# Optimization experiments

Measured on AMD Instinct MI355X. Metric: run time of the kernel, lower is better.

Reference implementation:

```python
import jax, jax.numpy as jnp
import numpy as np

WH, WW = 7, 7
SH, SW = 3, 3
NUM_HEADS = 8


def _rel_pos_index(wh, ww):
    coords = np.stack(np.meshgrid(np.arange(wh), np.arange(ww), indexing='ij')).reshape(2, -1)
    rel = (coords[:, :, None] - coords[:, None, :]).transpose(1, 2, 0)  # [N,N,2]
    rel[..., 0] += wh - 1
    rel[..., 1] += ww - 1
    rel[..., 0] *= 2 * ww - 1
    return rel.sum(-1)  # [N,N] int


def _attn_mask(Hp, Wp, wh, ww, sh, sw):
    img = np.zeros((Hp, Wp), dtype=np.float32)
    cnt = 0
    for hs in (slice(0, -wh), slice(-wh, -sh), slice(-sh, None)):
        for ws in (slice(0, -ww), slice(-ww, -sw), slice(-sw, None)):
            img[hs, ws] = cnt
            cnt += 1
    win = img.reshape(Hp // wh, wh, Wp // ww, ww).transpose(0, 2, 1, 3).reshape(-1, wh * ww)  # [nW,N]
    diff = win[:, None, :] - win[:, :, None]  # [nW,N,N]
    return np.where(diff != 0, -100.0, 0.0).astype(np.float32)


def _layernorm(x, g, b, eps=1e-5):
    mu = jnp.mean(x, -1, keepdims=True)
    var = jnp.mean(jnp.square(x - mu), -1, keepdims=True)
    return (x - mu) * jax.lax.rsqrt(var + eps) * g + b


def setup_inputs() -> dict:
    key = jax.random.key(0)
    ks = jax.random.split(key, 12)
    B, H, W, C = 32, 56, 56, 256
    hid = 4 * C
    s = lambda k, *shape: jax.random.normal(k, shape, jnp.float32) * 0.02
    return {
        'x': jax.random.normal(ks[0], (B, H * W, C), jnp.float32),
        'g1': jnp.ones((C,), jnp.float32), 'b1': jnp.zeros((C,), jnp.float32),
        'qkv_w': s(ks[1], 3 * C, C), 'qkv_b': jnp.zeros((3 * C,), jnp.float32),
        'bias_table': s(ks[2], (2 * WH - 1) * (2 * WW - 1), NUM_HEADS),
        'proj_w': s(ks[3], C, C), 'proj_b': jnp.zeros((C,), jnp.float32),
        'g2': jnp.ones((C,), jnp.float32), 'b2': jnp.zeros((C,), jnp.float32),
        'w1': s(ks[4], hid, C), 'bm1': jnp.zeros((hid,), jnp.float32),
        'w2': s(ks[5], C, hid), 'bm2': jnp.zeros((C,), jnp.float32),
        'H': H, 'W': W,
    }


def reference(x, g1, b1, qkv_w, qkv_b, bias_table, proj_w, proj_b, g2, b2, w1, bm1, w2, bm2, H, W):
    B, L, C = x.shape
    wh, ww = WH, WW
    nH = NUM_HEADS
    hd = C // nH
    scale = hd ** -0.5
    N = wh * ww

    shortcut = x
    h = _layernorm(x, g1, b1).reshape(B, H, W, C)
    pad_b = (wh - H % wh) % wh
    pad_r = (ww - W % ww) % ww
    if pad_b or pad_r:
        h = jnp.pad(h, ((0, 0), (0, pad_b), (0, pad_r), (0, 0)))
    Hp, Wp = h.shape[1], h.shape[2]

    h = jnp.roll(h, (-SH, -SW), axis=(1, 2))
    # window partition -> [B*nW, N, C]
    nWh, nWw = Hp // wh, Wp // ww
    xw = h.reshape(B, nWh, wh, nWw, ww, C).transpose(0, 1, 3, 2, 4, 5).reshape(-1, N, C)

    qkv = jnp.einsum('bnc,oc->bno', xw, qkv_w) + qkv_b  # [B*nW, N, 3C]
    qkv = qkv.reshape(-1, N, 3, nH, hd).transpose(2, 0, 3, 1, 4)
    q, k, v = qkv[0] * scale, qkv[1], qkv[2]  # [B*nW, nH, N, hd]
    attn = jnp.einsum('whnd,whmd->whnm', q, k)  # [B*nW, nH, N, N]

    rpi = jnp.asarray(_rel_pos_index(wh, ww))
    bias = bias_table[rpi.reshape(-1)].reshape(N, N, nH).transpose(2, 0, 1)  # [nH,N,N]
    attn = attn + bias[None]

    mask = jnp.asarray(_attn_mask(Hp, Wp, wh, ww, SH, SW))  # [nW,N,N]
    nW = mask.shape[0]
    attn = attn.reshape(B, nW, nH, N, N) + mask[None, :, None]
    attn = jax.nn.softmax(attn.reshape(-1, nH, N, N), axis=-1)

    out = jnp.einsum('whnm,whmd->whnd', attn, v).transpose(0, 2, 1, 3).reshape(-1, N, C)
    out = jnp.einsum('bnc,oc->bno', out, proj_w) + proj_b

    # window reverse
    out = out.reshape(B, nWh, nWw, wh, ww, C).transpose(0, 1, 3, 2, 4, 5).reshape(B, Hp, Wp, C)
    out = jnp.roll(out, (SH, SW), axis=(1, 2))
    if pad_b or pad_r:
        out = out[:, :H, :W, :]
    out = out.reshape(B, H * W, C)

    x = shortcut + out
    m = _layernorm(x, g2, b2)
    m = jax.nn.gelu(jnp.einsum('blc,oc->blo', m, w1) + bm1, approximate=False)
    m = jnp.einsum('blh,oh->blo', m, w2) + bm2
    return x + m
```

## Files before the change

kernel.cpp:

```cpp
#include <hip/hip_runtime.h>
#include <hip/hip_bf16.h>

#define DEVI __device__ __forceinline__
#define AS1 __attribute__((address_space(1)))
#define AS3 __attribute__((address_space(3)))

typedef short bf16x8 __attribute__((ext_vector_type(8)));
typedef float f32x4  __attribute__((ext_vector_type(4)));
typedef unsigned short u16x4 __attribute__((ext_vector_type(4)));

constexpr int MROWS = 100352;

DEVI int win_row_to_token(int r) {
  int b   = r / 3136;
  int rem = r - b * 3136;
  int wi  = rem / 49;
  int t   = rem - wi * 49;
  int nwh = wi >> 3, nww = wi & 7;
  int th = t / 7, tw = t - th * 7;
  int h = nwh * 7 + th + 3; if (h >= 56) h -= 56;
  int w = nww * 7 + tw + 3; if (w >= 56) w -= 56;
  return b * 3136 + h * 56 + w;
}

DEVI unsigned short f2bf(float f) {
  __hip_bfloat16 h = __float2bfloat16(f);
  return __builtin_bit_cast(unsigned short, h);
}

DEVI float gelu_t(float v) {
  float u2 = v * (1.5957691216f + 0.1426930877f * v * v);
  float e  = __expf(u2);
  return v * e / (e + 1.0f);
}

__global__ void pack_kernel(const float* __restrict__ W, __hip_bfloat16* __restrict__ Wp,
                            int N, int K) {
  long t = (long)blockIdx.x * 256 + threadIdx.x;
  long total = (long)N * K / 8;
  if (t >= total) return;
  int l  = (int)(t & 63);
  long f = t >> 6;
  int ni = (int)(f & 3);
  int kk = (int)((f >> 2) & 7);
  long r = f >> 5;
  int KB = K / 256;
  int kb = (int)(r % KB);
  int nb = (int)(r / KB);
  int row  = nb * 64 + (l & 15) + ni * 16;
  int col0 = kb * 256 + kk * 32 + (l >> 4) * 8;
  const float* src = W + (size_t)row * K + col0;
  u16x4 lo, hi;
  #pragma unroll
  for (int e = 0; e < 4; ++e) { lo[e] = f2bf(src[e]); hi[e] = f2bf(src[4 + e]); }
  *(u16x4*)(Wp + t * 8)     = lo;
  *(u16x4*)(Wp + t * 8 + 4) = hi;
}

__global__ __launch_bounds__(256) void ln_kernel(
    const float* __restrict__ xin, const float* __restrict__ g,
    const float* __restrict__ b, __hip_bfloat16* __restrict__ outb)
{
  int r = blockIdx.x * 4 + (threadIdx.x >> 6);
  int l = threadIdx.x & 63;
  int tok = win_row_to_token(r);
  float4 xv = *(const float4*)&xin[(size_t)tok * 256 + l * 4];
  float s = xv.x + xv.y + xv.z + xv.w;
  float q = xv.x * xv.x + xv.y * xv.y + xv.z * xv.z + xv.w * xv.w;
  #pragma unroll
  for (int off = 32; off; off >>= 1) { s += __shfl_xor(s, off); q += __shfl_xor(q, off); }
  float mu = s * (1.0f / 256.0f);
  float var = q * (1.0f / 256.0f) - mu * mu;
  float rs = rsqrtf(var + 1e-5f);
  float4 gv = *(const float4*)&g[l * 4];
  float4 bv = *(const float4*)&b[l * 4];
  ushort4 st;
  st.x = f2bf((xv.x - mu) * rs * gv.x + bv.x);
  st.y = f2bf((xv.y - mu) * rs * gv.y + bv.y);
  st.z = f2bf((xv.z - mu) * rs * gv.z + bv.z);
  st.w = f2bf((xv.w - mu) * rs * gv.w + bv.w);
  *(ushort4*)&outb[(size_t)r * 256 + l * 4] = st;
}

__global__ __launch_bounds__(256, 3) void gemm_qkv(
    const __hip_bfloat16* __restrict__ A,
    const __hip_bfloat16* __restrict__ Wp,
    const float* __restrict__ bias,
    __hip_bfloat16* __restrict__ outb)
{
  constexpr int CB = 3;
  __shared__ __align__(16) __hip_bfloat16 Al[64 * 256];

  const int tid = threadIdx.x;
  const int w = tid >> 6, l = tid & 63;
  const int g = l >> 4, lm = l & 15;

  const int nwg = gridDim.x;
  int bswz = (blockIdx.x & 7) * (nwg >> 3) + (blockIdx.x >> 3);
  const int mt = bswz / CB;
  const int cb = bswz - mt * CB;

  const char* At = (const char*)A + (size_t)mt * 64 * 512;
  char* AlB = (char*)Al;
  const int r0  = tid >> 5;
  const int usw = ((tid & 31) ^ r0) << 4;
  const int lmx = lm & 7;
  const int arow = lm * 512;

  const __hip_bfloat16* WpB = Wp + (size_t)(cb * 4 + w) * 16384;
  const int colb = cb * 256 + w * 64 + g * 4;

  f32x4 acc[4][4];
  {
    f32x4 bias_v[4];
    #pragma unroll
    for (int ni = 0; ni < 4; ++ni) bias_v[ni] = *(const f32x4*)&bias[colb + ni * 16];
    #pragma unroll
    for (int mi = 0; mi < 4; ++mi)
      #pragma unroll
      for (int ni = 0; ni < 4; ++ni) acc[mi][ni] = bias_v[ni];
  }

  #pragma unroll
  for (int j = 0; j < 8; ++j)
    __builtin_amdgcn_global_load_lds(
        (const AS1 void*)(At + (long)(j * 8 + r0) * 512 + usw),
        (AS3 void*)(AlB + j * 4096 + w * 1024), 16, 0, 0);
  asm volatile("s_waitcnt vmcnt(0)" ::: "memory");
  __syncthreads();

  #pragma unroll
  for (int kk = 0; kk < 8; ++kk) {
    bf16x8 bf[4], af[4];
    #pragma unroll
    for (int ni = 0; ni < 4; ++ni)
      bf[ni] = *(const bf16x8*)(WpB + ((kk * 4 + ni) * 64 + l) * 8);
    #pragma unroll
    for (int mi = 0; mi < 4; ++mi)
      af[mi] = *(const bf16x8*)(AlB + arow + mi * 8192 + ((((kk << 2) | g) ^ lmx) << 4));
    #pragma unroll
    for (int mi = 0; mi < 4; ++mi)
      #pragma unroll
      for (int ni = 0; ni < 4; ++ni)
        acc[mi][ni] = __builtin_amdgcn_mfma_f32_16x16x32_bf16(bf[ni], af[mi], acc[mi][ni], 0, 0, 0);
  }

  #pragma unroll
  for (int mi = 0; mi < 4; ++mi) {
    int grow = mt * 64 + mi * 16 + lm;
    __hip_bfloat16* rp = outb + (size_t)grow * 768 + colb;
    #pragma unroll
    for (int ni = 0; ni < 4; ++ni) {
      u16x4 st = { f2bf(acc[mi][ni][0]), f2bf(acc[mi][ni][1]),
                   f2bf(acc[mi][ni][2]), f2bf(acc[mi][ni][3]) };
      *(u16x4*)(rp + ni * 16) = st;
    }
  }
}

__global__ __launch_bounds__(256, 3) void proj_ln2(
    const __hip_bfloat16* __restrict__ A,
    const __hip_bfloat16* __restrict__ Wp,
    const float* __restrict__ bias,
    const float* __restrict__ xres,
    const float* __restrict__ g2, const float* __restrict__ b2,
    float* __restrict__ outf,
    __hip_bfloat16* __restrict__ alnout)
{
  __shared__ __align__(16) __hip_bfloat16 Al[64 * 256];
  __shared__ float2 Sst[4][16][4];

  const int tid = threadIdx.x;
  const int w = tid >> 6, l = tid & 63;
  const int g = l >> 4, lm = l & 15;

  const int nwg = gridDim.x;
  int bswz = (blockIdx.x & 7) * (nwg >> 3) + (blockIdx.x >> 3);
  const int mt = bswz;

  const char* At = (const char*)A + (size_t)mt * 64 * 512;
  char* AlB = (char*)Al;
  const int r0  = tid >> 5;
  const int usw = ((tid & 31) ^ r0) << 4;
  const int lmx = lm & 7;
  const int arow = lm * 512;

  const __hip_bfloat16* WpB = Wp + (size_t)w * 16384;
  const int colb = w * 64 + g * 4;

  f32x4 acc[4][4];
  {
    f32x4 bias_v[4];
    #pragma unroll
    for (int ni = 0; ni < 4; ++ni) bias_v[ni] = *(const f32x4*)&bias[colb + ni * 16];
    #pragma unroll
    for (int mi = 0; mi < 4; ++mi)
      #pragma unroll
      for (int ni = 0; ni < 4; ++ni) acc[mi][ni] = bias_v[ni];
  }

  #pragma unroll
  for (int j = 0; j < 8; ++j)
    __builtin_amdgcn_global_load_lds(
        (const AS1 void*)(At + (long)(j * 8 + r0) * 512 + usw),
        (AS3 void*)(AlB + j * 4096 + w * 1024), 16, 0, 0);
  asm volatile("s_waitcnt vmcnt(0)" ::: "memory");
  __syncthreads();

  #pragma unroll
  for (int kk = 0; kk < 8; ++kk) {
    bf16x8 bf[4], af[4];
    #pragma unroll
    for (int ni = 0; ni < 4; ++ni)
      bf[ni] = *(const bf16x8*)(WpB + ((kk * 4 + ni) * 64 + l) * 8);
    #pragma unroll
    for (int mi = 0; mi < 4; ++mi)
      af[mi] = *(const bf16x8*)(AlB + arow + mi * 8192 + ((((kk << 2) | g) ^ lmx) << 4));
    #pragma unroll
    for (int mi = 0; mi < 4; ++mi)
      #pragma unroll
      for (int ni = 0; ni < 4; ++ni)
        acc[mi][ni] = __builtin_amdgcn_mfma_f32_16x16x32_bf16(bf[ni], af[mi], acc[mi][ni], 0, 0, 0);
  }

  int orow_[4];
  #pragma unroll
  for (int mi = 0; mi < 4; ++mi) {
    int grow = mt * 64 + mi * 16 + lm;
    int orow = win_row_to_token(grow);
    orow_[mi] = orow;
    const f32x4* xr = (const f32x4*)(xres + (size_t)orow * 256 + colb);
    f32x4* op = (f32x4*)(outf + (size_t)orow * 256 + colb);
    float s = 0.0f, sq = 0.0f;
    #pragma unroll
    for (int ni = 0; ni < 4; ++ni) {
      f32x4 r = xr[ni * 4] + acc[mi][ni];
      acc[mi][ni] = r;
      op[ni * 4] = r;
      #pragma unroll
      for (int j = 0; j < 4; ++j) { s += r[j]; sq += r[j] * r[j]; }
    }
    s  += __shfl_xor(s, 16);  sq += __shfl_xor(sq, 16);
    s  += __shfl_xor(s, 32);  sq += __shfl_xor(sq, 32);
    if (g == 0) Sst[mi][lm][w] = float2{s, sq};
  }
  __syncthreads();

  f32x4 g2v[4], b2v[4];
  #pragma unroll
  for (int ni = 0; ni < 4; ++ni) {
    g2v[ni] = *(const f32x4*)&g2[colb + ni * 16];
    b2v[ni] = *(const f32x4*)&b2[colb + ni * 16];
  }
  #pragma unroll
  for (int mi = 0; mi < 4; ++mi) {
    float s = 0.0f, sq = 0.0f;
    #pragma unroll
    for (int ww = 0; ww < 4; ++ww) { float2 t = Sst[mi][lm][ww]; s += t.x; sq += t.y; }
    float mu = s * (1.0f / 256.0f);
    float rs = rsqrtf(sq * (1.0f / 256.0f) - mu * mu + 1e-5f);
    __hip_bfloat16* ap = alnout + (size_t)orow_[mi] * 256 + colb;
    #pragma unroll
    for (int ni = 0; ni < 4; ++ni) {
      u16x4 st;
      #pragma unroll
      for (int j = 0; j < 4; ++j)
        st[j] = f2bf((acc[mi][ni][j] - mu) * rs * g2v[ni][j] + b2v[ni][j]);
      *(u16x4*)(ap + ni * 16) = st;
    }
  }
}

__global__ __launch_bounds__(256, 1) void mlp_fused(
    const __hip_bfloat16* __restrict__ A,
    const __hip_bfloat16* __restrict__ W1p,
    const __hip_bfloat16* __restrict__ W2p,
    const float* __restrict__ bm1, const float* __restrict__ bm2,
    float* __restrict__ outf)
{
  __shared__ __align__(16) __hip_bfloat16 Al[64 * 256];
  __shared__ __align__(16) __hip_bfloat16 Hl[64 * 256];

  const int tid = threadIdx.x;
  const int w = tid >> 6, l = tid & 63;
  const int g = l >> 4, lm = l & 15;

  const int nwg = gridDim.x;
  int bswz = (blockIdx.x & 7) * (nwg >> 3) + (blockIdx.x >> 3);
  const int mt = bswz;

  const char* At = (const char*)A + (size_t)mt * 64 * 512;
  char* AlB = (char*)Al;
  char* HlB = (char*)Hl;
  const int usw = ((tid & 31) ^ ((tid >> 5) & 7)) << 4;
  const int lmx = lm & 7;
  const int arow = lm * 512;
  const int colb = w * 64 + g * 4;

  #pragma unroll
  for (int j = 0; j < 8; ++j)
    __builtin_amdgcn_global_load_lds(
        (const AS1 void*)(At + (long)(j * 8 + (tid >> 5)) * 512 + usw),
        (AS3 void*)(AlB + j * 4096 + w * 1024), 16, 0, 0);
  asm volatile("s_waitcnt vmcnt(0)" ::: "memory");
  __syncthreads();

  f32x4 acc2[4][4];
  {
    f32x4 b2v[4];
    #pragma unroll
    for (int ni = 0; ni < 4; ++ni) b2v[ni] = *(const f32x4*)&bm2[colb + ni * 16];
    #pragma unroll
    for (int mi = 0; mi < 4; ++mi)
      #pragma unroll
      for (int ni = 0; ni < 4; ++ni) acc2[mi][ni] = b2v[ni];
  }

  #pragma unroll
  for (int q = 0; q < 4; ++q) {
    const __hip_bfloat16* Wk1 = W1p + (size_t)(q * 4 + w) * 16384;
    const __hip_bfloat16* Wk2 = W2p + (size_t)(w * 4 + q) * 16384;

    f32x4 acc1[4][4];
    {
      f32x4 b1v[4];
      #pragma unroll
      for (int ni = 0; ni < 4; ++ni) b1v[ni] = *(const f32x4*)&bm1[q * 256 + colb + ni * 16];
      #pragma unroll
      for (int mi = 0; mi < 4; ++mi)
        #pragma unroll
        for (int ni = 0; ni < 4; ++ni) acc1[mi][ni] = b1v[ni];
    }
    bf16x8 bfc[4], afc[4], bfn[4], afn[4];
    #pragma unroll
    for (int ni = 0; ni < 4; ++ni)
      bfc[ni] = *(const bf16x8*)(Wk1 + (ni * 64 + l) * 8);
    #pragma unroll
    for (int mi = 0; mi < 4; ++mi)
      afc[mi] = *(const bf16x8*)(AlB + arow + mi * 8192 + ((g ^ lmx) << 4));
    #pragma unroll
    for (int kk = 0; kk < 8; ++kk) {
      if (kk < 7) {
        #pragma unroll
        for (int ni = 0; ni < 4; ++ni)
          bfn[ni] = *(const bf16x8*)(Wk1 + (((kk + 1) * 4 + ni) * 64 + l) * 8);
        #pragma unroll
        for (int mi = 0; mi < 4; ++mi)
          afn[mi] = *(const bf16x8*)(AlB + arow + mi * 8192 +
                                     (((((kk + 1) << 2) | g) ^ lmx) << 4));
      }
      #pragma unroll
      for (int mi = 0; mi < 4; ++mi)
        #pragma unroll
        for (int ni = 0; ni < 4; ++ni)
          acc1[mi][ni] = __builtin_amdgcn_mfma_f32_16x16x32_bf16(bfc[ni], afc[mi], acc1[mi][ni], 0, 0, 0);
      #pragma unroll
      for (int ni = 0; ni < 4; ++ni) bfc[ni] = bfn[ni];
      #pragma unroll
      for (int mi = 0; mi < 4; ++mi) afc[mi] = afn[mi];
    }

    #pragma unroll
    for (int ni = 0; ni < 4; ++ni)
      bfc[ni] = *(const bf16x8*)(Wk2 + (ni * 64 + l) * 8);

    __syncthreads();
    #pragma unroll
    for (int mi = 0; mi < 4; ++mi) {
      int rowb = (mi * 16 + lm) * 512;
      #pragma unroll
      for (int ni = 0; ni < 4; ++ni) {
        u16x4 hv = { f2bf(gelu_t(acc1[mi][ni][0])), f2bf(gelu_t(acc1[mi][ni][1])),
                     f2bf(gelu_t(acc1[mi][ni][2])), f2bf(gelu_t(acc1[mi][ni][3])) };
        int unit = (w * 8 + ni * 2 + (g >> 1)) ^ lmx;
        *(u16x4*)(HlB + rowb + unit * 16 + (g & 1) * 8) = hv;
      }
    }
    __syncthreads();

    #pragma unroll
    for (int mi = 0; mi < 4; ++mi)
      afc[mi] = *(const bf16x8*)(HlB + arow + mi * 8192 + ((g ^ lmx) << 4));
    #pragma unroll
    for (int kk = 0; kk < 8; ++kk) {
      if (kk < 7) {
        #pragma unroll
        for (int ni = 0; ni < 4; ++ni)
          bfn[ni] = *(const bf16x8*)(Wk2 + (((kk + 1) * 4 + ni) * 64 + l) * 8);
        #pragma unroll
        for (int mi = 0; mi < 4; ++mi)
          afn[mi] = *(const bf16x8*)(HlB + arow + mi * 8192 +
                                     (((((kk + 1) << 2) | g) ^ lmx) << 4));
      }
      #pragma unroll
      for (int mi = 0; mi < 4; ++mi)
        #pragma unroll
        for (int ni = 0; ni < 4; ++ni)
          acc2[mi][ni] = __builtin_amdgcn_mfma_f32_16x16x32_bf16(bfc[ni], afc[mi], acc2[mi][ni], 0, 0, 0);
      #pragma unroll
      for (int ni = 0; ni < 4; ++ni) bfc[ni] = bfn[ni];
      #pragma unroll
      for (int mi = 0; mi < 4; ++mi) afc[mi] = afn[mi];
    }
  }

  #pragma unroll
  for (int mi = 0; mi < 4; ++mi) {
    int grow = mt * 64 + mi * 16 + lm;
    f32x4* op = (f32x4*)(outf + (size_t)grow * 256 + colb);
    #pragma unroll
    for (int ni = 0; ni < 4; ++ni)
      op[ni * 4] = op[ni * 4] + acc2[mi][ni];
  }
}

__global__ __launch_bounds__(256) void bias_prep_kernel(
    const float* __restrict__ bt, float* __restrict__ Sadd)
{
  int blk = blockIdx.x;
  int cls = blk >> 3, h = blk & 7;
  int re = cls >> 1, ce = cls & 1;
  int lane = threadIdx.x & 63, fs = threadIdx.x >> 6;
  int g = lane >> 4, lm = lane & 15;
  #pragma unroll
  for (int i = 0; i < 4; ++i) {
    int f = fs * 4 + i;
    int mi = f >> 2, ni = f & 3;
    int key = ni * 16 + lm;
    f32x4 v;
    #pragma unroll
    for (int j = 0; j < 4; ++j) {
      int q = mi * 16 + g * 4 + j;
      float val;
      if (key >= 49) {
        val = -1e30f;
      } else {
        int qq = q > 48 ? 48 : q;
        int qh = qq / 7, qw = qq - qh * 7;
        int kh = key / 7, kw = key - kh * 7;
        int rpi = (qh - kh + 6) * 13 + (qw - kw + 6);
        val = bt[rpi * 8 + h];
        int rq = (re ? (qh < 4 ? 1 : 2) : 0) * 3 + (ce ? (qw < 4 ? 1 : 2) : 0);
        int rk = (re ? (kh < 4 ? 1 : 2) : 0) * 3 + (ce ? (kw < 4 ? 1 : 2) : 0);
        if (rq != rk) val -= 100.0f;
      }
      v[j] = val;
    }
    ((f32x4*)Sadd)[(blk * 16 + f) * 64 + lane] = v;
  }
}

__global__ __launch_bounds__(256) void attn_mfma_kernel(
    const __hip_bfloat16* __restrict__ qkv,
    const float* __restrict__ Sadd,
    __hip_bfloat16* __restrict__ attn_out)
{
  __shared__ __align__(16) __hip_bfloat16 Pl[4][64 * 72];
  int blk = blockIdx.x;
  int win = blk >> 1, half = blk & 1;
  int w = threadIdx.x >> 6, l = threadIdx.x & 63;
  int head = half * 4 + w;
  int g = l >> 4, lm = l & 15;
  int wi = win & 63;
  int cls = (((wi >> 3) == 7) ? 2 : 0) | (((wi & 7) == 7) ? 1 : 0);
  const __hip_bfloat16* base = qkv + (size_t)win * 49 * 768 + head * 32;

  bf16x8 aQ[4], bK[4];
  #pragma unroll
  for (int mi = 0; mi < 4; ++mi) {
    int q = mi * 16 + lm; if (q > 48) q = 48;
    aQ[mi] = *(const bf16x8*)(base + q * 768 + g * 8);
  }
  #pragma unroll
  for (int ni = 0; ni < 4; ++ni) {
    int k = ni * 16 + lm; if (k > 48) k = 48;
    bK[ni] = *(const bf16x8*)(base + 256 + k * 768 + g * 8);
  }
  f32x4 acc[4][4] = {};
  #pragma unroll
  for (int mi = 0; mi < 4; ++mi)
    #pragma unroll
    for (int ni = 0; ni < 4; ++ni)
      acc[mi][ni] = __builtin_amdgcn_mfma_f32_16x16x32_bf16(aQ[mi], bK[ni], acc[mi][ni], 0, 0, 0);

  const float scale = 0.17677669529663687f;
  const f32x4* Sb = (const f32x4*)Sadd + (size_t)(cls * 8 + head) * 16 * 64 + l;

  f32x4 rsum[4];
  __hip_bfloat16* P = Pl[w];
  #pragma unroll
  for (int mi = 0; mi < 4; ++mi) {
    #pragma unroll
    for (int ni = 0; ni < 4; ++ni) {
      f32x4 sv = Sb[(mi * 4 + ni) * 64];
      #pragma unroll
      for (int j = 0; j < 4; ++j) acc[mi][ni][j] = acc[mi][ni][j] * scale + sv[j];
    }
    f32x4 mx = acc[mi][0];
    #pragma unroll
    for (int ni = 1; ni < 4; ++ni)
      #pragma unroll
      for (int j = 0; j < 4; ++j) mx[j] = fmaxf(mx[j], acc[mi][ni][j]);
    #pragma unroll
    for (int msk = 1; msk < 16; msk <<= 1)
      #pragma unroll
      for (int j = 0; j < 4; ++j) mx[j] = fmaxf(mx[j], __shfl_xor(mx[j], msk));
    f32x4 sm = {};
    #pragma unroll
    for (int ni = 0; ni < 4; ++ni)
      #pragma unroll
      for (int j = 0; j < 4; ++j) {
        float e = __expf(acc[mi][ni][j] - mx[j]);
        acc[mi][ni][j] = e;
        sm[j] += e;
      }
    #pragma unroll
    for (int msk = 1; msk < 16; msk <<= 1)
      #pragma unroll
      for (int j = 0; j < 4; ++j) sm[j] += __shfl_xor(sm[j], msk);
    rsum[mi] = sm;
    #pragma unroll
    for (int ni = 0; ni < 4; ++ni)
      #pragma unroll
      for (int j = 0; j < 4; ++j) {
        int q = mi * 16 + g * 4 + j;
        int key = ni * 16 + lm;
        P[q * 72 + key] = __float2bfloat16(acc[mi][ni][j]);
      }
  }

  bf16x8 bV[2][2];
  #pragma unroll
  for (int s = 0; s < 2; ++s)
    #pragma unroll
    for (int n2 = 0; n2 < 2; ++n2) {
      bf16x8 vv;
      #pragma unroll
      for (int e = 0; e < 8; ++e) {
        int key = s * 32 + g * 8 + e; if (key > 48) key = 48;
        vv[e] = __builtin_bit_cast(short, base[512 + key * 768 + n2 * 16 + lm]);
      }
      bV[s][n2] = vv;
    }

  f32x4 o[4][2] = {};
  #pragma unroll
  for (int s = 0; s < 2; ++s)
    #pragma unroll
    for (int mi2 = 0; mi2 < 4; ++mi2) {
      bf16x8 aP = *(const bf16x8*)&P[(mi2 * 16 + lm) * 72 + s * 32 + g * 8];
      #pragma unroll
      for (int n2 = 0; n2 < 2; ++n2)
        o[mi2][n2] = __builtin_amdgcn_mfma_f32_16x16x32_bf16(aP, bV[s][n2], o[mi2][n2], 0, 0, 0);
    }

  #pragma unroll
  for (int mi2 = 0; mi2 < 4; ++mi2) {
    f32x4 li;
    #pragma unroll
    for (int j = 0; j < 4; ++j) li[j] = 1.0f / rsum[mi2][j];
    #pragma unroll
    for (int n2 = 0; n2 < 2; ++n2)
      #pragma unroll
      for (int j = 0; j < 4; ++j) {
        int q = mi2 * 16 + g * 4 + j;
        if (q < 49)
          attn_out[((size_t)win * 49 + q) * 256 + head * 32 + n2 * 16 + lm] =
              __float2bfloat16(o[mi2][n2][j] * li[j]);
      }
  }
}

extern "C" void kernel_launch(void* const* d_in, const int* in_sizes, int n_in,
                              void* d_out, int out_size, void* d_ws, size_t ws_size,
                              hipStream_t stream) {
  const float* x          = (const float*)d_in[0];
  const float* g1         = (const float*)d_in[1];
  const float* b1         = (const float*)d_in[2];
  const float* qkv_w      = (const float*)d_in[3];
  const float* qkv_b      = (const float*)d_in[4];
  const float* bias_table = (const float*)d_in[5];
  const float* proj_w     = (const float*)d_in[6];
  const float* proj_b     = (const float*)d_in[7];
  const float* g2         = (const float*)d_in[8];
  const float* b2         = (const float*)d_in[9];
  const float* w1         = (const float*)d_in[10];
  const float* bm1        = (const float*)d_in[11];
  const float* w2         = (const float*)d_in[12];
  const float* bm2        = (const float*)d_in[13];
  float* out = (float*)d_out;

  char* ws = (char*)d_ws;
  __hip_bfloat16* A_ln   = (__hip_bfloat16*)(ws);
  __hip_bfloat16* qkvb   = (__hip_bfloat16*)(ws + 51380224);
  __hip_bfloat16* attn_o = (__hip_bfloat16*)(ws + 205520896);
  __hip_bfloat16* qkv_wb  = (__hip_bfloat16*)(ws + 256901120);
  __hip_bfloat16* proj_wb = qkv_wb + 196608;
  __hip_bfloat16* w1b     = proj_wb + 65536;
  __hip_bfloat16* w2b     = w1b + 262144;
  float* Sadd = (float*)(ws + 258473984);

  pack_kernel<<<(196608 / 8 + 255) / 256, 256, 0, stream>>>(qkv_w, qkv_wb, 768, 256);
  pack_kernel<<<(65536  / 8 + 255) / 256, 256, 0, stream>>>(proj_w, proj_wb, 256, 256);
  pack_kernel<<<(262144 / 8 + 255) / 256, 256, 0, stream>>>(w1, w1b, 1024, 256);
  pack_kernel<<<(262144 / 8 + 255) / 256, 256, 0, stream>>>(w2, w2b, 256, 1024);
  bias_prep_kernel<<<32, 256, 0, stream>>>(bias_table, Sadd);

  ln_kernel<<<MROWS / 4, 256, 0, stream>>>(x, g1, b1, A_ln);

  gemm_qkv<<<1568 * 3, 256, 0, stream>>>(A_ln, qkv_wb, qkv_b, qkvb);

  attn_mfma_kernel<<<4096, 256, 0, stream>>>(qkvb, Sadd, attn_o);

  proj_ln2<<<1568, 256, 0, stream>>>(attn_o, proj_wb, proj_b, x, g2, b2, out, A_ln);

  mlp_fused<<<1568, 256, 0, stream>>>(A_ln, w1b, w2b, bm1, bm2, out);
}
```

Baseline: 454.4 us.

## Fuse LayerNorm1 into QKV GEMM and loop over all column blocks per tile

Removes the standalone LayerNorm kernel. The QKV GEMM now loads fp32 rows directly, normalizes them, and writes swizzled bf16 into LDS. Each workgroup then loops over all three 256-column blocks, so the A tile is staged once instead of three times, and the grid shrinks to 1568 blocks. This avoids writing and reading the bf16 A_ln intermediate, but the LN prologue is serial per wave and is not overlapped with compute. Occupancy drops to 2 waves per SIMD per the launch bounds, and there are fewer blocks on the GPU.

```diff
diff --git a/kernel.cpp b/kernel.cpp
--- a/kernel.cpp
+++ b/kernel.cpp
@@ -57,38 +57,13 @@
   *(u16x4*)(Wp + t * 8 + 4) = hi;
 }
 
-__global__ __launch_bounds__(256) void ln_kernel(
-    const float* __restrict__ xin, const float* __restrict__ g,
-    const float* __restrict__ b, __hip_bfloat16* __restrict__ outb)
-{
-  int r = blockIdx.x * 4 + (threadIdx.x >> 6);
-  int l = threadIdx.x & 63;
-  int tok = win_row_to_token(r);
-  float4 xv = *(const float4*)&xin[(size_t)tok * 256 + l * 4];
-  float s = xv.x + xv.y + xv.z + xv.w;
-  float q = xv.x * xv.x + xv.y * xv.y + xv.z * xv.z + xv.w * xv.w;
-  #pragma unroll
-  for (int off = 32; off; off >>= 1) { s += __shfl_xor(s, off); q += __shfl_xor(q, off); }
-  float mu = s * (1.0f / 256.0f);
-  float var = q * (1.0f / 256.0f) - mu * mu;
-  float rs = rsqrtf(var + 1e-5f);
-  float4 gv = *(const float4*)&g[l * 4];
-  float4 bv = *(const float4*)&b[l * 4];
-  ushort4 st;
-  st.x = f2bf((xv.x - mu) * rs * gv.x + bv.x);
-  st.y = f2bf((xv.y - mu) * rs * gv.y + bv.y);
-  st.z = f2bf((xv.z - mu) * rs * gv.z + bv.z);
-  st.w = f2bf((xv.w - mu) * rs * gv.w + bv.w);
-  *(ushort4*)&outb[(size_t)r * 256 + l * 4] = st;
-}
-
-__global__ __launch_bounds__(256, 3) void gemm_qkv(
-    const __hip_bfloat16* __restrict__ A,
+__global__ __launch_bounds__(256, 2) void gemm_qkv_ln(
+    const float* __restrict__ x,
     const __hip_bfloat16* __restrict__ Wp,
     const float* __restrict__ bias,
+    const float* __restrict__ g1, const float* __restrict__ b1,
     __hip_bfloat16* __restrict__ outb)
 {
-  constexpr int CB = 3;
   __shared__ __align__(16) __hip_bfloat16 Al[64 * 256];
 
   const int tid = threadIdx.x;
@@ -97,63 +72,77 @@
 
   const int nwg = gridDim.x;
   int bswz = (blockIdx.x & 7) * (nwg >> 3) + (blockIdx.x >> 3);
-  const int mt = bswz / CB;
-  const int cb = bswz - mt * CB;
-
-  const char* At = (const char*)A + (size_t)mt * 64 * 512;
+  const int mt = bswz;
+
   char* AlB = (char*)Al;
-  const int r0  = tid >> 5;
-  const int usw = ((tid & 31) ^ r0) << 4;
   const int lmx = lm & 7;
   const int arow = lm * 512;
 
-  const __hip_bfloat16* WpB = Wp + (size_t)(cb * 4 + w) * 16384;
-  const int colb = cb * 256 + w * 64 + g * 4;
-
-  f32x4 acc[4][4];
   {
-    f32x4 bias_v[4];
-    #pragma unroll
-    for (int ni = 0; ni < 4; ++ni) bias_v[ni] = *(const f32x4*)&bias[colb + ni * 16];
-    #pragma unroll
-    for (int mi = 0; mi < 4; ++mi)
-      #pragma unroll
-      for (int ni = 0; ni < 4; ++ni) acc[mi][ni] = bias_v[ni];
-  }
-
-  #pragma unroll
-  for (int j = 0; j < 8; ++j)
-    __builtin_amdgcn_global_load_lds(
-        (const AS1 void*)(At + (long)(j * 8 + r0) * 512 + usw),
-        (AS3 void*)(AlB + j * 4096 + w * 1024), 16, 0, 0);
-  asm volatile("s_waitcnt vmcnt(0)" ::: "memory");
+    float4 gv = *(const float4*)&g1[l * 4];
+    float4 bv = *(const float4*)&b1[l * 4];
+    for (int rr = 0; rr < 16; ++rr) {
+      int row = w * 16 + rr;
+      int tok = win_row_to_token(mt * 64 + row);
+      float4 xv = *(const float4*)&x[(size_t)tok * 256 + l * 4];
+      float s = xv.x + xv.y + xv.z + xv.w;
+      float q = xv.x * xv.x + xv.y * xv.y + xv.z * xv.z + xv.w * xv.w;
+      #pragma unroll
+      for (int off = 32; off; off >>= 1) { s += __shfl_xor(s, off); q += __shfl_xor(q, off); }
+      float mu = s * (1.0f / 256.0f);
+      float var = q * (1.0f / 256.0f) - mu * mu;
+      float rs = rsqrtf(var + 1e-5f);
+      u16x4 st;
+      st[0] = f2bf((xv.x - mu) * rs * gv.x + bv.x);
+      st[1] = f2bf((xv.y - mu) * rs * gv.y + bv.y);
+      st[2] = f2bf((xv.z - mu) * rs * gv.z + bv.z);
+      st[3] = f2bf((xv.w - mu) * rs * gv.w + bv.w);
+      *(u16x4*)(AlB + row * 512 + (((l >> 1) ^ (row & 7)) << 4) + (l & 1) * 8) = st;
+    }
+  }
   __syncthreads();
 
-  #pragma unroll
-  for (int kk = 0; kk < 8; ++kk) {
-    bf16x8 bf[4], af[4];
-    #pragma unroll
-    for (int ni = 0; ni < 4; ++ni)
-      bf[ni] = *(const bf16x8*)(WpB + ((kk * 4 + ni) * 64 + l) * 8);
-    #pragma unroll
-    for (int mi = 0; mi < 4; ++mi)
-      af[mi] = *(const bf16x8*)(AlB + arow + mi * 8192 + ((((kk << 2) | g) ^ lmx) << 4));
-    #pragma unroll
-    for (int mi = 0; mi < 4; ++mi)
+  for (int cb = 0; cb < 3; ++cb) {
+    const __hip_bfloat16* WpB = Wp + (size_t)(cb * 4 + w) * 16384;
+    const int colb = cb * 256 + w * 64 + g * 4;
+
+    f32x4 acc[4][4];
+    {
+      f32x4 bias_v[4];
+      #pragma unroll
+      for (int ni = 0; ni < 4; ++ni) bias_v[ni] = *(const f32x4*)&bias[colb + ni * 16];
+      #pragma unroll
+      for (int mi = 0; mi < 4; ++mi)
+        #pragma unroll
+        for (int ni = 0; ni < 4; ++ni) acc[mi][ni] = bias_v[ni];
+    }
+
+    #pragma unroll
+    for (int kk = 0; kk < 8; ++kk) {
+      bf16x8 bf[4], af[4];
       #pragma unroll
       for (int ni = 0; ni < 4; ++ni)
-        acc[mi][ni] = __builtin_amdgcn_mfma_f32_16x16x32_bf16(bf[ni], af[mi], acc[mi][ni], 0, 0, 0);
-  }
-
-  #pragma unroll
-  for (int mi = 0; mi < 4; ++mi) {
-    int grow = mt * 64 + mi * 16 + lm;
-    __hip_bfloat16* rp = outb + (size_t)grow * 768 + colb;
-    #pragma unroll
-    for (int ni = 0; ni < 4; ++ni) {
-      u16x4 st = { f2bf(acc[mi][ni][0]), f2bf(acc[mi][ni][1]),
-                   f2bf(acc[mi][ni][2]), f2bf(acc[mi][ni][3]) };
-      *(u16x4*)(rp + ni * 16) = st;
+        bf[ni] = *(const bf16x8*)(WpB + ((kk * 4 + ni) * 64 + l) * 8);
+      #pragma unroll
+      for (int mi = 0; mi < 4; ++mi)
+        af[mi] = *(const bf16x8*)(AlB + arow + mi * 8192 + ((((kk << 2) | g) ^ lmx) << 4));
+      #pragma unroll
+      for (int mi = 0; mi < 4; ++mi)
+        #pragma unroll
+        for (int ni = 0; ni < 4; ++ni)
+          acc[mi][ni] = __builtin_amdgcn_mfma_f32_16x16x32_bf16(bf[ni], af[mi], acc[mi][ni], 0, 0, 0);
+    }
+
+    #pragma unroll
+    for (int mi = 0; mi < 4; ++mi) {
+      int grow = mt * 64 + mi * 16 + lm;
+      __hip_bfloat16* rp = outb + (size_t)grow * 768 + colb;
+      #pragma unroll
+      for (int ni = 0; ni < 4; ++ni) {
+        u16x4 st = { f2bf(acc[mi][ni][0]), f2bf(acc[mi][ni][1]),
+                     f2bf(acc[mi][ni][2]), f2bf(acc[mi][ni][3]) };
+        *(u16x4*)(rp + ni * 16) = st;
+      }
     }
   }
 }
@@ -606,9 +595,7 @@
   pack_kernel<<<(262144 / 8 + 255) / 256, 256, 0, stream>>>(w2, w2b, 256, 1024);
   bias_prep_kernel<<<32, 256, 0, stream>>>(bias_table, Sadd);
 
-  ln_kernel<<<MROWS / 4, 256, 0, stream>>>(x, g1, b1, A_ln);
-
-  gemm_qkv<<<1568 * 3, 256, 0, stream>>>(A_ln, qkv_wb, qkv_b, qkvb);
+  gemm_qkv_ln<<<1568, 256, 0, stream>>>(x, qkv_wb, qkv_b, g1, b1, qkvb);
 
   attn_mfma_kernel<<<4096, 256, 0, stream>>>(qkvb, Sadd, attn_o);
 
```

Result: slower. 499.5 us (+9.9%).
